# Kernel tuning notes

Measured on AMD Instinct MI355X. Metric: run time of the kernel, lower is better.

The kernel has to match this reference:

```python
import jax, jax.numpy as jnp
import numpy as np

C = 512
NUM_HEADS = 8
NUM_GROUPS = 32
EPS = 1e-6


def group_norm(x, gamma, beta):
    # x: [B, C, N]
    b, c, n = x.shape
    xg = x.reshape(b, NUM_GROUPS, (c // NUM_GROUPS) * n)
    mean = xg.mean(axis=-1, keepdims=True)
    var = xg.var(axis=-1, keepdims=True)
    xg = (xg - mean) * jax.lax.rsqrt(var + EPS)
    x = xg.reshape(b, c, n)
    return x * gamma[None, :, None] + beta[None, :, None]


def conv1x1(x, w, bias):
    # pointwise conv: w [out_c, in_c], x [B, C, N]
    return jnp.einsum('oc,bcn->bon', w, x) + bias[None, :, None]


def setup_inputs() -> dict:
    key = jax.random.key(0)
    ks = jax.random.split(key, 11)
    s = 1.0 / np.sqrt(C)
    inp = {
        'x': jax.random.normal(ks[0], (4, C, 2048), dtype=jnp.float32),
        'gn_gamma': jnp.ones((C,), jnp.float32),
        'gn_beta': jnp.zeros((C,), jnp.float32),
        'q_w': jax.random.uniform(ks[1], (C, C), jnp.float32, -s, s),
        'q_b': jax.random.uniform(ks[2], (C,), jnp.float32, -s, s),
        'k_w': jax.random.uniform(ks[3], (C, C), jnp.float32, -s, s),
        'k_b': jax.random.uniform(ks[4], (C,), jnp.float32, -s, s),
        'v_w': jax.random.uniform(ks[5], (C, C), jnp.float32, -s, s),
        'v_b': jax.random.uniform(ks[6], (C,), jnp.float32, -s, s),
        'proj_w': jax.random.uniform(ks[7], (C, C), jnp.float32, -s, s),
        'proj_b': jax.random.uniform(ks[8], (C,), jnp.float32, -s, s),
    }
    return inp


def reference(x, gn_gamma, gn_beta, q_w, q_b, k_w, k_b, v_w, v_b, proj_w, proj_b):
    b, c, n = x.shape
    hc = c // NUM_HEADS
    h_ = group_norm(x, gn_gamma, gn_beta)
    q = conv1x1(h_, q_w, q_b)
    k = conv1x1(h_, k_w, k_b)
    v = conv1x1(h_, v_w, v_b)
    # split heads: [B, H, hc, N]
    q = q.reshape(b, NUM_HEADS, hc, n)
    k = k.reshape(b, NUM_HEADS, hc, n)
    v = v.reshape(b, NUM_HEADS, hc, n)
    # NOTE: scale uses full channel count c, matching the original code
    scale = jnp.asarray(c, x.dtype) ** -0.5
    # scores: [B, H, Nq, Nk]
    w = jnp.einsum('bhcn,bhcm->bhnm', q, k) * scale
    w = jax.nn.softmax(w, axis=-1)
    # out[b,h,c,q] = sum_m v[b,h,c,m] * w[b,h,q,m]
    out = jnp.einsum('bhcm,bhqm->bhcq', v, w)
    out = out.reshape(b, c, n)
    out = conv1x1(out, proj_w, proj_b)
    return x + out
```

## Files before the change

kernel.cpp:

```cpp
#include <hip/hip_runtime.h>
#include <hip/hip_bf16.h>
#include <math.h>

#define C_DIM 512
#define N_DIM 2048
#define B_DIM 4
#define NGRP 32
#define GCH 16
#define NHEAD 8
#define HDIM 64
#define EPSV 1e-6f

using f32x4  = __attribute__((ext_vector_type(4))) float;
using bf16x8 = __attribute__((ext_vector_type(8))) short;

#define GLL16(gp, lp) __builtin_amdgcn_global_load_lds( \
    (const __attribute__((address_space(1))) unsigned int*)(gp), \
    (__attribute__((address_space(3))) unsigned int*)(lp), 16, 0, 0)

static __device__ __forceinline__ unsigned short f2bf(float f) {
    union { __hip_bfloat16 h; unsigned short u; } cv;
    cv.h = __float2bfloat16(f);
    return cv.u;
}

__global__ __launch_bounds__(256) void gn_stats(const float* __restrict__ x,
                                                float* __restrict__ stats) {
    const int GSZ = GCH * N_DIM;
    int bg = blockIdx.x;
    const float4* x4 = (const float4*)(x + (size_t)bg * GSZ);
    int tid = threadIdx.x;

    float s = 0.f, ss = 0.f;
    #pragma unroll
    for (int it = 0; it < GSZ / 4 / 256; ++it) {
        float4 v = x4[tid + it * 256];
        s  += v.x + v.y + v.z + v.w;
        ss += v.x * v.x + v.y * v.y + v.z * v.z + v.w * v.w;
    }
    __shared__ float rs[256], rss[256];
    rs[tid] = s; rss[tid] = ss;
    __syncthreads();
    for (int off = 128; off > 0; off >>= 1) {
        if (tid < off) { rs[tid] += rs[tid + off]; rss[tid] += rss[tid + off]; }
        __syncthreads();
    }
    if (tid == 0) {
        float mean = rs[0] * (1.f / GSZ);
        float var  = rss[0] * (1.f / GSZ) - mean * mean;
        stats[bg * 2]     = mean;
        stats[bg * 2 + 1] = rsqrtf(var + EPSV);
    }
}

__global__ __launch_bounds__(256) void gn_apply_t(const float* __restrict__ x,
                                                  const float* __restrict__ stats,
                                                  const float* __restrict__ gamma,
                                                  const float* __restrict__ beta,
                                                  unsigned short* __restrict__ ht) {
    __shared__ char smem[8192];
    int n0 = blockIdx.x * 64, c0 = blockIdx.y * 64, b = blockIdx.z;
    int tid = threadIdx.x;
    #pragma unroll
    for (int it = 0; it < 4; ++it) {
        int idx = tid + it * 256;
        int ci = idx >> 4, n4 = (idx & 15) << 2;
        int cg = c0 + ci, grp = cg >> 4;
        float mean = stats[(b * NGRP + grp) * 2];
        float rstd = stats[(b * NGRP + grp) * 2 + 1];
        float ga = gamma[cg] * rstd, be = beta[cg] - mean * ga;
        float4 v = *(const float4*)&x[((size_t)b * C_DIM + cg) * N_DIM + n0 + n4];
        float vals[4] = {v.x, v.y, v.z, v.w};
        #pragma unroll
        for (int j = 0; j < 4; ++j) {
            int nl = n4 + j;
            *(unsigned short*)(smem + nl * 128 + ((ci * 2) ^ ((nl & 7) << 4))) =
                f2bf(vals[j] * ga + be);
        }
    }
    __syncthreads();
    #pragma unroll
    for (int i = 0; i < 2; ++i) {
        int idx = tid + i * 256;
        int row = idx >> 3, ch = idx & 7;
        bf16x8 v = *(const bf16x8*)(smem + row * 128 + ((ch * 16) ^ ((row & 7) << 4)));
        *(bf16x8*)&ht[((size_t)(b * N_DIM + n0 + row)) * C_DIM + c0 + ch * 8] = v;
    }
}

__global__ __launch_bounds__(256) void cast4_bf16(const float* __restrict__ s0,
                                                  const float* __restrict__ s1,
                                                  const float* __restrict__ s2,
                                                  const float* __restrict__ s3,
                                                  unsigned short* __restrict__ dst) {
    int which = blockIdx.y;
    const float* src = (which == 0) ? s0 : (which == 1) ? s1 : (which == 2) ? s2 : s3;
    size_t idx = (size_t)blockIdx.x * 256 + threadIdx.x;
    const float4* s4 = (const float4*)src;
    float4 a = s4[idx * 2], b = s4[idx * 2 + 1];
    bf16x8 o;
    o[0] = (short)f2bf(a.x); o[1] = (short)f2bf(a.y);
    o[2] = (short)f2bf(a.z); o[3] = (short)f2bf(a.w);
    o[4] = (short)f2bf(b.x); o[5] = (short)f2bf(b.y);
    o[6] = (short)f2bf(b.z); o[7] = (short)f2bf(b.w);
    *(bf16x8*)&dst[(size_t)which * 262144 + idx * 8] = o;
}

template <int MODE>
__global__ __launch_bounds__(256) void conv_mfma(const unsigned short* __restrict__ Wb,
                                                 const float* __restrict__ bias,
                                                 const unsigned short* __restrict__ Bsrc,
                                                 const float* __restrict__ res,
                                                 void* __restrict__ outp,
                                                 float escale) {
    __shared__ char smem[24576];
    unsigned short* As = (unsigned short*)smem;
    unsigned short* Bs = (unsigned short*)(smem + 8192);

    int bn0 = blockIdx.x * 128;
    int bo  = blockIdx.y * 64;
    int tid = threadIdx.x;
    int L = tid & 63, w = tid >> 6;
    int g = L >> 4, c = L & 15;
    int wr = w >> 1, wc = w & 1;

    f32x4 acc[2][4];
    #pragma unroll
    for (int t = 0; t < 2; ++t)
        #pragma unroll
        for (int u = 0; u < 4; ++u) acc[t][u] = f32x4{0.f, 0.f, 0.f, 0.f};

    for (int k0 = 0; k0 < C_DIM; k0 += 64) {
        #pragma unroll
        for (int i = 0; i < 2; ++i) {
            int j = w * 2 + i;
            int ra = j * 8 + (L >> 3);
            int sl = (L & 7) ^ (ra & 7);
            GLL16(Wb + (size_t)(bo + ra) * C_DIM + k0 + sl * 8, (char*)As + j * 1024);
        }
        #pragma unroll
        for (int i = 0; i < 4; ++i) {
            int j = w * 4 + i;
            int rb = j * 8 + (L >> 3);
            int sl = (L & 7) ^ (rb & 7);
            GLL16(Bsrc + (size_t)(bn0 + rb) * C_DIM + k0 + sl * 8, (char*)Bs + j * 1024);
        }
        __syncthreads();

        bf16x8 af[2][2], bfr[4][2];
        #pragma unroll
        for (int t = 0; t < 2; ++t) {
            int row = wr * 32 + t * 16 + c;
            #pragma unroll
            for (int ks = 0; ks < 2; ++ks)
                af[t][ks] = *(const bf16x8*)((char*)As + row * 128 +
                                             ((g * 16 + ks * 64) ^ ((row & 7) << 4)));
        }
        #pragma unroll
        for (int u = 0; u < 4; ++u) {
            int row = wc * 64 + u * 16 + c;
            #pragma unroll
            for (int ks = 0; ks < 2; ++ks)
                bfr[u][ks] = *(const bf16x8*)((char*)Bs + row * 128 +
                                              ((g * 16 + ks * 64) ^ ((row & 7) << 4)));
        }
        #pragma unroll
        for (int ks = 0; ks < 2; ++ks)
            #pragma unroll
            for (int t = 0; t < 2; ++t)
                #pragma unroll
                for (int u = 0; u < 4; ++u)
                    acc[t][u] = __builtin_amdgcn_mfma_f32_16x16x32_bf16(
                        af[t][ks], bfr[u][ks], acc[t][u], 0, 0, 0);
        __syncthreads();
    }

    int b  = bn0 >> 11;
    int nb = bn0 & (N_DIM - 1);

    if (MODE == 0) {
        unsigned short* vt = (unsigned short*)outp;
        #pragma unroll
        for (int t = 0; t < 2; ++t)
            #pragma unroll
            for (int r = 0; r < 4; ++r) {
                int m = bo + wr * 32 + t * 16 + g * 4 + r;
                float bi = bias[m];
                #pragma unroll
                for (int u = 0; u < 4; ++u) {
                    int n = nb + wc * 64 + u * 16 + c;
                    vt[((size_t)b * C_DIM + m) * N_DIM + n] = f2bf(acc[t][u][r] + bi);
                }
            }
    } else if (MODE == 1) {
        int hh = bo >> 6;
        int bh = b * NHEAD + hh;
        unsigned short* Ts = (unsigned short*)smem;
        __syncthreads();
        #pragma unroll
        for (int t = 0; t < 2; ++t)
            #pragma unroll
            for (int r = 0; r < 4; ++r) {
                int ml = wr * 32 + t * 16 + g * 4 + r;
                float bi = bias[bo + ml];
                #pragma unroll
                for (int u = 0; u < 4; ++u) {
                    int nl = wc * 64 + u * 16 + c;
                    *(unsigned short*)((char*)Ts + nl * 128 + ((ml * 2) ^ ((nl & 7) << 4))) =
                        f2bf((acc[t][u][r] + bi) * escale);
                }
            }
        __syncthreads();
        unsigned short* qt = (unsigned short*)outp;
        #pragma unroll
        for (int i = 0; i < 4; ++i) {
            int idx = tid + i * 256;
            int row = idx >> 3, ch = idx & 7;
            bf16x8 v = *(const bf16x8*)((char*)Ts + row * 128 + ((ch * 16) ^ ((row & 7) << 4)));
            *(bf16x8*)&qt[((size_t)bh * N_DIM + nb + row) * HDIM + ch * 8] = v;
        }
    } else {
        float* outf = (float*)outp;
        #pragma unroll
        for (int t = 0; t < 2; ++t)
            #pragma unroll
            for (int r = 0; r < 4; ++r) {
                int m = bo + wr * 32 + t * 16 + g * 4 + r;
                float bi = bias[m];
                #pragma unroll
                for (int u = 0; u < 4; ++u) {
                    int n = nb + wc * 64 + u * 16 + c;
                    size_t off = ((size_t)b * C_DIM + m) * N_DIM + n;
                    outf[off] = acc[t][u][r] + bi + res[off];
                }
            }
    }
}

__global__ __launch_bounds__(512, 4) void attn_kernel(const unsigned short* __restrict__ Qt,
                                                      const unsigned short* __restrict__ Kt,
                                                      const unsigned short* __restrict__ Vt,
                                                      unsigned short* __restrict__ at) {
    __shared__ char smem[49152];
    char* PQ = smem;

    int q0 = blockIdx.x * 128;
    int bh = blockIdx.y;
    int b = bh >> 3, hh = bh & 7;
    int tid = threadIdx.x;
    int L = tid & 63, w = tid >> 6;
    int g = L >> 4, c = L & 15;

    const unsigned short* Qh = Qt + (size_t)bh * N_DIM * HDIM;
    const unsigned short* Kh = Kt + (size_t)bh * N_DIM * HDIM;
    const unsigned short* Vh = Vt + (size_t)bh * HDIM * N_DIM;

    #pragma unroll
    for (int i = 0; i < 2; ++i) {
        int j = w * 2 + i;
        int row = j * 8 + (L >> 3);
        int sl = (L & 7) ^ (row & 7);
        GLL16(Qh + (size_t)(q0 + row) * HDIM + sl * 8, PQ + j * 1024);
    }
    {
        int row = w * 8 + (L >> 3);
        int sl = (L & 7) ^ (row & 7);
        GLL16(Kh + (size_t)row * HDIM + sl * 8, smem + 16384 + w * 1024);
        GLL16(Vh + (size_t)row * N_DIM + sl * 8, smem + 24576 + w * 1024);
    }
    __syncthreads();

    int prow = w * 16 + c;
    int psw = (c & 7) << 4;
    char* pb = PQ + prow * 128;
    bf16x8 qf[2];
    #pragma unroll
    for (int ks = 0; ks < 2; ++ks)
        qf[ks] = *(const bf16x8*)(pb + ((g * 16 + ks * 64) ^ psw));

    f32x4 oacc[4];
    #pragma unroll
    for (int t = 0; t < 4; ++t) oacc[t] = f32x4{0.f, 0.f, 0.f, 0.f};
    float m_r = -INFINITY, l_r = 0.f;

    for (int kt = 0; kt < N_DIM / 64; ++kt) {
        int cur = kt & 1;
        char* Ksb = smem + 16384 + cur * 16384;
        char* Vsb = Ksb + 8192;
        if (kt < N_DIM / 64 - 1) {
            int k0n = (kt + 1) * 64;
            int row = w * 8 + (L >> 3);
            int sl = (L & 7) ^ (row & 7);
            char* Ksn = smem + 16384 + (cur ^ 1) * 16384;
            GLL16(Kh + (size_t)(k0n + row) * HDIM + sl * 8, Ksn + w * 1024);
            GLL16(Vh + (size_t)row * N_DIM + k0n + sl * 8, Ksn + 8192 + w * 1024);
        }

        f32x4 sacc[4];
        #pragma unroll
        for (int t = 0; t < 4; ++t) sacc[t] = f32x4{0.f, 0.f, 0.f, 0.f};
        __builtin_amdgcn_s_setprio(1);
        #pragma unroll
        for (int t = 0; t < 4; ++t) {
            int row = t * 16 + c;
            #pragma unroll
            for (int ks = 0; ks < 2; ++ks) {
                bf16x8 kf = *(const bf16x8*)(Ksb + row * 128 +
                                             ((g * 16 + ks * 64) ^ ((row & 7) << 4)));
                sacc[t] = __builtin_amdgcn_mfma_f32_16x16x32_bf16(kf, qf[ks], sacc[t], 0, 0, 0);
            }
        }
        __builtin_amdgcn_s_setprio(0);

        float mloc = fmaxf(
            fmaxf(fmaxf(fmaxf(sacc[0][0], sacc[0][1]), fmaxf(sacc[0][2], sacc[0][3])),
                  fmaxf(fmaxf(sacc[1][0], sacc[1][1]), fmaxf(sacc[1][2], sacc[1][3]))),
            fmaxf(fmaxf(fmaxf(sacc[2][0], sacc[2][1]), fmaxf(sacc[2][2], sacc[2][3])),
                  fmaxf(fmaxf(sacc[3][0], sacc[3][1]), fmaxf(sacc[3][2], sacc[3][3]))));
        mloc = fmaxf(mloc, __shfl_xor(mloc, 16));
        mloc = fmaxf(mloc, __shfl_xor(mloc, 32));
        if (!__all(mloc - m_r <= 6.0f)) {
            float mn = fmaxf(m_r, mloc);
            float fac = exp2f(m_r - mn);
            m_r = mn;
            l_r *= fac;
            #pragma unroll
            for (int t = 0; t < 4; ++t) oacc[t] = oacc[t] * fac;
        }
        float rs = 0.f;
        unsigned pk[4][2];
        #pragma unroll
        for (int t = 0; t < 4; ++t) {
            float p0 = exp2f(sacc[t][0] - m_r);
            float p1 = exp2f(sacc[t][1] - m_r);
            float p2 = exp2f(sacc[t][2] - m_r);
            float p3 = exp2f(sacc[t][3] - m_r);
            rs += (p0 + p1) + (p2 + p3);
            pk[t][0] = (unsigned)f2bf(p0) | ((unsigned)f2bf(p1) << 16);
            pk[t][1] = (unsigned)f2bf(p2) | ((unsigned)f2bf(p3) << 16);
        }
        rs += __shfl_xor(rs, 16);
        rs += __shfl_xor(rs, 32);
        l_r += rs;

        #pragma unroll
        for (int t = 0; t < 4; ++t)
            *(unsigned long long*)(pb + ((t * 32 + g * 8) ^ psw)) =
                (unsigned long long)pk[t][0] | ((unsigned long long)pk[t][1] << 32);

        __builtin_amdgcn_s_setprio(1);
        #pragma unroll
        for (int ks = 0; ks < 2; ++ks) {
            bf16x8 pf = *(const bf16x8*)(pb + ((ks * 64 + g * 16) ^ psw));
            #pragma unroll
            for (int t = 0; t < 4; ++t) {
                int vrow = t * 16 + c;
                bf16x8 vf = *(const bf16x8*)(Vsb + vrow * 128 +
                                             ((g * 16 + ks * 64) ^ ((vrow & 7) << 4)));
                oacc[t] = __builtin_amdgcn_mfma_f32_16x16x32_bf16(vf, pf, oacc[t], 0, 0, 0);
            }
        }
        __builtin_amdgcn_s_setprio(0);

        __syncthreads();
    }

    float oinv = 1.f / l_r;
    #pragma unroll
    for (int t = 0; t < 4; ++t) {
        unsigned lo = (unsigned)f2bf(oacc[t][0] * oinv) |
                      ((unsigned)f2bf(oacc[t][1] * oinv) << 16);
        unsigned hi = (unsigned)f2bf(oacc[t][2] * oinv) |
                      ((unsigned)f2bf(oacc[t][3] * oinv) << 16);
        *(unsigned long long*)(pb + ((t * 32 + g * 8) ^ psw)) =
            (unsigned long long)lo | ((unsigned long long)hi << 32);
    }
    char* wbase = PQ + w * 2048;
    #pragma unroll
    for (int i = 0; i < 2; ++i) {
        int idx = L + i * 64;
        int row = idx >> 3, ch = idx & 7;
        bf16x8 v = *(const bf16x8*)(wbase + row * 128 + ((ch * 16) ^ ((row & 7) << 4)));
        *(bf16x8*)&at[((size_t)(b * N_DIM + q0 + w * 16 + row)) * C_DIM + hh * HDIM + ch * 8] = v;
    }
}

extern "C" void kernel_launch(void* const* d_in, const int* in_sizes, int n_in,
                              void* d_out, int out_size, void* d_ws, size_t ws_size,
                              hipStream_t stream) {
    (void)in_sizes; (void)n_in; (void)out_size; (void)ws_size;
    const float* x     = (const float*)d_in[0];
    const float* gam   = (const float*)d_in[1];
    const float* bet   = (const float*)d_in[2];
    const float* q_w   = (const float*)d_in[3];
    const float* q_b   = (const float*)d_in[4];
    const float* k_w   = (const float*)d_in[5];
    const float* k_b   = (const float*)d_in[6];
    const float* v_w   = (const float*)d_in[7];
    const float* v_b   = (const float*)d_in[8];
    const float* p_w   = (const float*)d_in[9];
    const float* p_b   = (const float*)d_in[10];
    float* out = (float*)d_out;

    const size_t MB = 1 << 20;
    char* wsb = (char*)d_ws;
    unsigned short* ht  = (unsigned short*)(wsb);
    unsigned short* wqb = (unsigned short*)(wsb + 8 * MB);
    unsigned short* wkb = (unsigned short*)(wsb + 8 * MB + 512 * 1024);
    unsigned short* wvb = (unsigned short*)(wsb + 9 * MB);
    unsigned short* wpb = (unsigned short*)(wsb + 9 * MB + 512 * 1024);
    float*          stats = (float*)(wsb + 10 * MB);
    unsigned short* qt  = (unsigned short*)(wsb + 11 * MB);
    unsigned short* kt  = (unsigned short*)(wsb + 19 * MB);
    unsigned short* vt  = (unsigned short*)(wsb + 27 * MB);
    unsigned short* at  = (unsigned short*)(wsb + 35 * MB);

    gn_stats<<<B_DIM * NGRP, 256, 0, stream>>>(x, stats);
    gn_apply_t<<<dim3(N_DIM / 64, C_DIM / 64, B_DIM), 256, 0, stream>>>(x, stats, gam, bet, ht);

    cast4_bf16<<<dim3(128, 4), 256, 0, stream>>>(q_w, k_w, v_w, p_w, wqb);

    const float escale = 0.044194173824159216f * 1.4426950408889634f;
    dim3 cgrid(B_DIM * N_DIM / 128, C_DIM / 64);
    conv_mfma<1><<<cgrid, 256, 0, stream>>>(wqb, q_b, ht, nullptr, qt, escale);
    conv_mfma<1><<<cgrid, 256, 0, stream>>>(wkb, k_b, ht, nullptr, kt, 1.0f);
    conv_mfma<0><<<cgrid, 256, 0, stream>>>(wvb, v_b, ht, nullptr, vt, 1.0f);

    attn_kernel<<<dim3(N_DIM / 128, B_DIM * NHEAD), 512, 0, stream>>>(qt, kt, vt, at);

    conv_mfma<2><<<cgrid, 256, 0, stream>>>(wpb, p_b, at, x, out, 1.0f);
}
```

Baseline: 125.3 us.

## Fuse Q/K/V pointwise convs into one kernel sharing activation tiles

Replaces three separate Q, K and V conv launches with a single kernel that loads each activation tile once and multiplies it against all three weight tiles, with one wave per source doing the LDS staging. The N tile shrinks to 64 to keep registers and LDS manageable. This cuts two launches and two redundant reads of the normalized activations. It also swaps the bf16 conversion in attention for a byte-permute truncation pack, which drops round-to-nearest and may change numerics slightly, and reshuffles the max reduction tree.

```diff
diff --git a/kernel.cpp b/kernel.cpp
--- a/kernel.cpp
+++ b/kernel.cpp
@@ -17,6 +17,8 @@
 #define GLL16(gp, lp) __builtin_amdgcn_global_load_lds( \
     (const __attribute__((address_space(1))) unsigned int*)(gp), \
     (__attribute__((address_space(3))) unsigned int*)(lp), 16, 0, 0)
+
+#define BFPACK(a, b) __builtin_amdgcn_perm(__float_as_uint(b), __float_as_uint(a), 0x07060302u)
 
 static __device__ __forceinline__ unsigned short f2bf(float f) {
     union { __hip_bfloat16 h; unsigned short u; } cv;
@@ -106,17 +108,134 @@
     *(bf16x8*)&dst[(size_t)which * 262144 + idx * 8] = o;
 }
 
-template <int MODE>
-__global__ __launch_bounds__(256) void conv_mfma(const unsigned short* __restrict__ Wb,
+__global__ __launch_bounds__(256) void conv_qkv(const unsigned short* __restrict__ Wall,
+                                                const float* __restrict__ q_b,
+                                                const float* __restrict__ k_b,
+                                                const float* __restrict__ v_b,
+                                                const unsigned short* __restrict__ ht,
+                                                unsigned short* __restrict__ qt,
+                                                unsigned short* __restrict__ kt,
+                                                unsigned short* __restrict__ vt,
+                                                float escale) {
+    __shared__ char smem[32768];
+
+    int bn0 = blockIdx.x * 64;
+    int bo  = blockIdx.y * 64;
+    int tid = threadIdx.x;
+    int L = tid & 63, w = tid >> 6;
+    int g = L >> 4, c = L & 15;
+    int wr = w >> 1, wc = w & 1;
+
+    f32x4 acc[3][2][2];
+    #pragma unroll
+    for (int w3 = 0; w3 < 3; ++w3)
+        #pragma unroll
+        for (int t = 0; t < 2; ++t)
+            #pragma unroll
+            for (int u = 0; u < 2; ++u) acc[w3][t][u] = f32x4{0.f, 0.f, 0.f, 0.f};
+
+    const unsigned short* sbase;
+    char* ldsb;
+    if (w == 0) { sbase = ht + (size_t)bn0 * C_DIM; ldsb = smem; }
+    else { sbase = Wall + (size_t)(w - 1) * 262144 + (size_t)bo * C_DIM; ldsb = smem + w * 8192; }
+
+    for (int k0 = 0; k0 < C_DIM; k0 += 64) {
+        #pragma unroll
+        for (int i = 0; i < 8; ++i) {
+            int row = i * 8 + (L >> 3);
+            int sl = (L & 7) ^ (row & 7);
+            GLL16(sbase + (size_t)row * C_DIM + k0 + sl * 8, ldsb + i * 1024);
+        }
+        __syncthreads();
+
+        bf16x8 bfr[2][2];
+        #pragma unroll
+        for (int u = 0; u < 2; ++u) {
+            int row = wc * 32 + u * 16 + c;
+            #pragma unroll
+            for (int ks = 0; ks < 2; ++ks)
+                bfr[u][ks] = *(const bf16x8*)(smem + row * 128 +
+                                              ((g * 16 + ks * 64) ^ ((row & 7) << 4)));
+        }
+        #pragma unroll
+        for (int w3 = 0; w3 < 3; ++w3) {
+            char* As = smem + 8192 + w3 * 8192;
+            bf16x8 af[2][2];
+            #pragma unroll
+            for (int t = 0; t < 2; ++t) {
+                int row = wr * 32 + t * 16 + c;
+                #pragma unroll
+                for (int ks = 0; ks < 2; ++ks)
+                    af[t][ks] = *(const bf16x8*)(As + row * 128 +
+                                                 ((g * 16 + ks * 64) ^ ((row & 7) << 4)));
+            }
+            #pragma unroll
+            for (int ks = 0; ks < 2; ++ks)
+                #pragma unroll
+                for (int t = 0; t < 2; ++t)
+                    #pragma unroll
+                    for (int u = 0; u < 2; ++u)
+                        acc[w3][t][u] = __builtin_amdgcn_mfma_f32_16x16x32_bf16(
+                            af[t][ks], bfr[u][ks], acc[w3][t][u], 0, 0, 0);
+        }
+        __syncthreads();
+    }
+
+    int b  = bn0 >> 11;
+    int nb = bn0 & (N_DIM - 1);
+    int hh = bo >> 6;
+    int bh = b * NHEAD + hh;
+
+    #pragma unroll
+    for (int t = 0; t < 2; ++t)
+        #pragma unroll
+        for (int r = 0; r < 4; ++r) {
+            int m = bo + wr * 32 + t * 16 + g * 4 + r;
+            float bi = v_b[m];
+            #pragma unroll
+            for (int u = 0; u < 2; ++u) {
+                int n = nb + wc * 32 + u * 16 + c;
+                vt[((size_t)b * C_DIM + m) * N_DIM + n] = f2bf(acc[2][t][u][r] + bi);
+            }
+        }
+
+    char* Ts = smem;
+    #pragma unroll
+    for (int pass = 0; pass < 2; ++pass) {
+        const float* bias = pass ? k_b : q_b;
+        float esc = pass ? 1.0f : escale;
+        unsigned short* dst = pass ? kt : qt;
+        __syncthreads();
+        #pragma unroll
+        for (int t = 0; t < 2; ++t)
+            #pragma unroll
+            for (int r = 0; r < 4; ++r) {
+                int ml = wr * 32 + t * 16 + g * 4 + r;
+                float bi = bias[bo + ml];
+                #pragma unroll
+                for (int u = 0; u < 2; ++u) {
+                    int nl = wc * 32 + u * 16 + c;
+                    *(unsigned short*)(Ts + nl * 128 + ((ml * 2) ^ ((nl & 7) << 4))) =
+                        f2bf((acc[pass][t][u][r] + bi) * esc);
+                }
+            }
+        __syncthreads();
+        #pragma unroll
+        for (int i = 0; i < 2; ++i) {
+            int idx = tid + i * 256;
+            int row = idx >> 3, ch = idx & 7;
+            bf16x8 v = *(const bf16x8*)(Ts + row * 128 + ((ch * 16) ^ ((row & 7) << 4)));
+            *(bf16x8*)&dst[((size_t)bh * N_DIM + nb + row) * HDIM + ch * 8] = v;
+        }
+    }
+}
+
+__global__ __launch_bounds__(256) void conv_proj(const unsigned short* __restrict__ Wb,
                                                  const float* __restrict__ bias,
                                                  const unsigned short* __restrict__ Bsrc,
                                                  const float* __restrict__ res,
-                                                 void* __restrict__ outp,
-                                                 float escale) {
+                                                 float* __restrict__ outf) {
     __shared__ char smem[24576];
-    unsigned short* As = (unsigned short*)smem;
-    unsigned short* Bs = (unsigned short*)(smem + 8192);
-
     int bn0 = blockIdx.x * 128;
     int bo  = blockIdx.y * 64;
     int tid = threadIdx.x;
@@ -136,14 +255,14 @@
             int j = w * 2 + i;
             int ra = j * 8 + (L >> 3);
             int sl = (L & 7) ^ (ra & 7);
-            GLL16(Wb + (size_t)(bo + ra) * C_DIM + k0 + sl * 8, (char*)As + j * 1024);
+            GLL16(Wb + (size_t)(bo + ra) * C_DIM + k0 + sl * 8, smem + j * 1024);
         }
         #pragma unroll
         for (int i = 0; i < 4; ++i) {
             int j = w * 4 + i;
             int rb = j * 8 + (L >> 3);
             int sl = (L & 7) ^ (rb & 7);
-            GLL16(Bsrc + (size_t)(bn0 + rb) * C_DIM + k0 + sl * 8, (char*)Bs + j * 1024);
+            GLL16(Bsrc + (size_t)(bn0 + rb) * C_DIM + k0 + sl * 8, smem + 8192 + j * 1024);
         }
         __syncthreads();
 
@@ -153,7 +272,7 @@
             int row = wr * 32 + t * 16 + c;
             #pragma unroll
             for (int ks = 0; ks < 2; ++ks)
-                af[t][ks] = *(const bf16x8*)((char*)As + row * 128 +
+                af[t][ks] = *(const bf16x8*)(smem + row * 128 +
                                              ((g * 16 + ks * 64) ^ ((row & 7) << 4)));
         }
         #pragma unroll
@@ -161,7 +280,7 @@
             int row = wc * 64 + u * 16 + c;
             #pragma unroll
             for (int ks = 0; ks < 2; ++ks)
-                bfr[u][ks] = *(const bf16x8*)((char*)Bs + row * 128 +
+                bfr[u][ks] = *(const bf16x8*)(smem + 8192 + row * 128 +
                                               ((g * 16 + ks * 64) ^ ((row & 7) << 4)));
         }
         #pragma unroll
@@ -177,64 +296,19 @@
 
     int b  = bn0 >> 11;
     int nb = bn0 & (N_DIM - 1);
-
-    if (MODE == 0) {
-        unsigned short* vt = (unsigned short*)outp;
-        #pragma unroll
-        for (int t = 0; t < 2; ++t)
-            #pragma unroll
-            for (int r = 0; r < 4; ++r) {
-                int m = bo + wr * 32 + t * 16 + g * 4 + r;
-                float bi = bias[m];
-                #pragma unroll
-                for (int u = 0; u < 4; ++u) {
-                    int n = nb + wc * 64 + u * 16 + c;
-                    vt[((size_t)b * C_DIM + m) * N_DIM + n] = f2bf(acc[t][u][r] + bi);
-                }
+    #pragma unroll
+    for (int t = 0; t < 2; ++t)
+        #pragma unroll
+        for (int r = 0; r < 4; ++r) {
+            int m = bo + wr * 32 + t * 16 + g * 4 + r;
+            float bi = bias[m];
+            #pragma unroll
+            for (int u = 0; u < 4; ++u) {
+                int n = nb + wc * 64 + u * 16 + c;
+                size_t off = ((size_t)b * C_DIM + m) * N_DIM + n;
+                outf[off] = acc[t][u][r] + bi + res[off];
             }
-    } else if (MODE == 1) {
-        int hh = bo >> 6;
-        int bh = b * NHEAD + hh;
-        unsigned short* Ts = (unsigned short*)smem;
-        __syncthreads();
-        #pragma unroll
-        for (int t = 0; t < 2; ++t)
-            #pragma unroll
-            for (int r = 0; r < 4; ++r) {
-                int ml = wr * 32 + t * 16 + g * 4 + r;
-                float bi = bias[bo + ml];
-                #pragma unroll
-                for (int u = 0; u < 4; ++u) {
-                    int nl = wc * 64 + u * 16 + c;
-                    *(unsigned short*)((char*)Ts + nl * 128 + ((ml * 2) ^ ((nl & 7) << 4))) =
-                        f2bf((acc[t][u][r] + bi) * escale);
-                }
-            }
-        __syncthreads();
-        unsigned short* qt = (unsigned short*)outp;
-        #pragma unroll
-        for (int i = 0; i < 4; ++i) {
-            int idx = tid + i * 256;
-            int row = idx >> 3, ch = idx & 7;
-            bf16x8 v = *(const bf16x8*)((char*)Ts + row * 128 + ((ch * 16) ^ ((row & 7) << 4)));
-            *(bf16x8*)&qt[((size_t)bh * N_DIM + nb + row) * HDIM + ch * 8] = v;
-        }
-    } else {
-        float* outf = (float*)outp;
-        #pragma unroll
-        for (int t = 0; t < 2; ++t)
-            #pragma unroll
-            for (int r = 0; r < 4; ++r) {
-                int m = bo + wr * 32 + t * 16 + g * 4 + r;
-                float bi = bias[m];
-                #pragma unroll
-                for (int u = 0; u < 4; ++u) {
-                    int n = nb + wc * 64 + u * 16 + c;
-                    size_t off = ((size_t)b * C_DIM + m) * N_DIM + n;
-                    outf[off] = acc[t][u][r] + bi + res[off];
-                }
-            }
-    }
+        }
 }
 
 __global__ __launch_bounds__(512, 4) void attn_kernel(const unsigned short* __restrict__ Qt,
@@ -312,11 +386,14 @@
         }
         __builtin_amdgcn_s_setprio(0);
 
-        float mloc = fmaxf(
-            fmaxf(fmaxf(fmaxf(sacc[0][0], sacc[0][1]), fmaxf(sacc[0][2], sacc[0][3])),
-                  fmaxf(fmaxf(sacc[1][0], sacc[1][1]), fmaxf(sacc[1][2], sacc[1][3]))),
-            fmaxf(fmaxf(fmaxf(sacc[2][0], sacc[2][1]), fmaxf(sacc[2][2], sacc[2][3])),
-                  fmaxf(fmaxf(sacc[3][0], sacc[3][1]), fmaxf(sacc[3][2], sacc[3][3]))));
+        float t0 = fmaxf(fmaxf(sacc[0][0], sacc[0][1]), sacc[0][2]);
+        float t1 = fmaxf(fmaxf(sacc[0][3], sacc[1][0]), sacc[1][1]);
+        float t2 = fmaxf(fmaxf(sacc[1][2], sacc[1][3]), sacc[2][0]);
+        float t3 = fmaxf(fmaxf(sacc[2][1], sacc[2][2]), sacc[2][3]);
+        float t4 = fmaxf(fmaxf(sacc[3][0], sacc[3][1]), sacc[3][2]);
+        float u0 = fmaxf(fmaxf(t0, t1), t2);
+        float u1 = fmaxf(fmaxf(t3, t4), sacc[3][3]);
+        float mloc = fmaxf(u0, u1);
         mloc = fmaxf(mloc, __shfl_xor(mloc, 16));
         mloc = fmaxf(mloc, __shfl_xor(mloc, 32));
         if (!__all(mloc - m_r <= 6.0f)) {
@@ -336,8 +413,8 @@
             float p2 = exp2f(sacc[t][2] - m_r);
             float p3 = exp2f(sacc[t][3] - m_r);
             rs += (p0 + p1) + (p2 + p3);
-            pk[t][0] = (unsigned)f2bf(p0) | ((unsigned)f2bf(p1) << 16);
-            pk[t][1] = (unsigned)f2bf(p2) | ((unsigned)f2bf(p3) << 16);
+            pk[t][0] = BFPACK(p0, p1);
+            pk[t][1] = BFPACK(p2, p3);
         }
         rs += __shfl_xor(rs, 16);
         rs += __shfl_xor(rs, 32);
@@ -368,10 +445,8 @@
     float oinv = 1.f / l_r;
     #pragma unroll
     for (int t = 0; t < 4; ++t) {
-        unsigned lo = (unsigned)f2bf(oacc[t][0] * oinv) |
-                      ((unsigned)f2bf(oacc[t][1] * oinv) << 16);
-        unsigned hi = (unsigned)f2bf(oacc[t][2] * oinv) |
-                      ((unsigned)f2bf(oacc[t][3] * oinv) << 16);
+        unsigned lo = BFPACK(oacc[t][0] * oinv, oacc[t][1] * oinv);
+        unsigned hi = BFPACK(oacc[t][2] * oinv, oacc[t][3] * oinv);
         *(unsigned long long*)(pb + ((t * 32 + g * 8) ^ psw)) =
             (unsigned long long)lo | ((unsigned long long)hi << 32);
     }
@@ -406,8 +481,6 @@
     char* wsb = (char*)d_ws;
     unsigned short* ht  = (unsigned short*)(wsb);
     unsigned short* wqb = (unsigned short*)(wsb + 8 * MB);
-    unsigned short* wkb = (unsigned short*)(wsb + 8 * MB + 512 * 1024);
-    unsigned short* wvb = (unsigned short*)(wsb + 9 * MB);
     unsigned short* wpb = (unsigned short*)(wsb + 9 * MB + 512 * 1024);
     float*          stats = (float*)(wsb + 10 * MB);
     unsigned short* qt  = (unsigned short*)(wsb + 11 * MB);
@@ -421,12 +494,10 @@
     cast4_bf16<<<dim3(128, 4), 256, 0, stream>>>(q_w, k_w, v_w, p_w, wqb);
 
     const float escale = 0.044194173824159216f * 1.4426950408889634f;
-    dim3 cgrid(B_DIM * N_DIM / 128, C_DIM / 64);
-    conv_mfma<1><<<cgrid, 256, 0, stream>>>(wqb, q_b, ht, nullptr, qt, escale);
-    conv_mfma<1><<<cgrid, 256, 0, stream>>>(wkb, k_b, ht, nullptr, kt, 1.0f);
-    conv_mfma<0><<<cgrid, 256, 0, stream>>>(wvb, v_b, ht, nullptr, vt, 1.0f);
+    conv_qkv<<<dim3(B_DIM * N_DIM / 64, C_DIM / 64), 256, 0, stream>>>(
+        wqb, q_b, k_b, v_b, ht, qt, kt, vt, escale);
 
     attn_kernel<<<dim3(N_DIM / 128, B_DIM * NHEAD), 512, 0, stream>>>(qt, kt, vt, at);
 
-    conv_mfma<2><<<cgrid, 256, 0, stream>>>(wpb, p_b, at, x, out, 1.0f);
-}
+    conv_proj<<<dim3(B_DIM * N_DIM / 128, C_DIM / 64), 256, 0, stream>>>(wpb, p_b, at, x, out);
+}
```

Result: faster. 121.2 us (-3.3%).
